# Optimization experiments

Measured on AMD Instinct MI355X. Metric: run time of the kernel, lower is better.

## Reference

```python
import jax, jax.numpy as jnp
import numpy as np

N, V, E_PER = 8, 4608, 73728          # batch, nodes per graph, edges per graph
D_IN, C, NCLS = 1, 512, 3             # node feat dim, embed dim, classes
E = N * E_PER
LN_EPS = 1e-5


def setup_inputs() -> dict:
    key = jax.random.key(0)
    ks = jax.random.split(key, 12)
    x = jax.random.normal(ks[0], (N, 1, V, D_IN), jnp.float32)
    edge_index = jax.random.randint(ks[1], (2, E), 0, V, dtype=jnp.int32)
    edge_weight = jax.random.uniform(ks[2], (E,), jnp.float32)
    # GCNConv params: layer0 maps D_IN->C, layers 1..2 map C->C (weight [in,out], bias [out])
    w0 = jax.random.normal(ks[3], (D_IN, C), jnp.float32) * 0.02
    b0 = jnp.zeros((C,), jnp.float32)
    w1 = jax.random.normal(ks[4], (C, C), jnp.float32) * 0.02
    b1 = jnp.zeros((C,), jnp.float32)
    w2 = jax.random.normal(ks[5], (C, C), jnp.float32) * 0.02
    b2 = jnp.zeros((C,), jnp.float32)
    ln_g = jnp.ones((C,), jnp.float32)
    ln_b = jnp.zeros((C,), jnp.float32)
    head_w = jax.random.normal(ks[6], (C, NCLS), jnp.float32) * 2e-5
    head_b = jnp.log(jnp.full((NCLS,), 1.0 / NCLS, jnp.float32))
    return {"x": x, "edge_weight": edge_weight, "w0": w0, "b0": b0,
            "w1": w1, "b1": b1, "w2": w2, "b2": b2,
            "ln_g": ln_g, "ln_b": ln_b, "head_w": head_w, "head_b": head_b,
            "edge_index": edge_index}


def layer_norm(h, g, b):
    mu = h.mean(-1, keepdims=True)
    var = ((h - mu) ** 2).mean(-1, keepdims=True)
    return (h - mu) * jax.lax.rsqrt(var + LN_EPS) * g + b


def reference(x, edge_weight, w0, b0, w1, b1, w2, b2, ln_g, ln_b, head_w, head_b, edge_index):
    n, t, v, d = x.shape
    nv = n * v
    h = x.reshape(nv, d)
    # batch-offset local edge indices (edges are contiguous per graph)
    offs = jnp.repeat(jnp.arange(n, dtype=edge_index.dtype) * v, edge_index.shape[1] // n)
    src = edge_index[0] + offs
    tgt = edge_index[1] + offs
    # GCN norm with self-loops (fill weight 1.0), symmetric deg^-1/2 normalization
    loop = jnp.arange(nv, dtype=src.dtype)
    src_f = jnp.concatenate([src, loop])
    tgt_f = jnp.concatenate([tgt, loop])
    ew_f = jnp.concatenate([edge_weight, jnp.ones((nv,), edge_weight.dtype)])
    deg = jax.ops.segment_sum(ew_f, tgt_f, num_segments=nv)
    deg_safe = jnp.where(deg > 0, deg, 1.0)
    dinv = jnp.where(deg > 0, jax.lax.rsqrt(deg_safe), 0.0)
    norm = dinv[src_f] * ew_f * dinv[tgt_f]
    for w, bb in ((w0, b0), (w1, b1), (w2, b2)):
        hw = h @ w                                   # [NV, C]
        msg = norm[:, None] * hw[src_f]              # gather + scale  [E+NV, C]
        h = jax.ops.segment_sum(msg, tgt_f, num_segments=nv) + bb
        h = jax.nn.relu(h)
        h = layer_norm(h, ln_g, ln_b)
        # dropout is identity in eval mode
    pooled = h.reshape(n, v, -1).max(axis=1)         # global_max_pool (contiguous batch)
    pooled = layer_norm(pooled, ln_g, ln_b)
    return pooled @ head_w + head_b                  # [N, NCLS]
```

## Files before the change

kernel.cpp:

```cpp
#include <hip/hip_runtime.h>
#include <hip/hip_bf16.h>
#include <stdint.h>

#define N_GRAPH 8
#define V_NODES 4608
#define E_PER   73728
#define NV      (N_GRAPH * V_NODES)
#define E_TOT   (N_GRAPH * E_PER)
#define C       512
#define NCLS    3
#define LN_EPS  1e-5f
#define POOL_CHUNKS 36
#define POOL_PARTS  144
#define SCAN_BLOCKS 144
#define SUBB    32
#define EPSB    (E_PER / SUBB)

typedef __attribute__((ext_vector_type(8))) short short8;
typedef __attribute__((ext_vector_type(4))) float floatx4;
typedef __attribute__((ext_vector_type(2))) float float2v;
typedef __attribute__((address_space(1))) void v_g;
typedef __attribute__((address_space(3))) void v_l;


__device__ inline float waveReduceSum(float v) {
#pragma unroll
    for (int o = 32; o > 0; o >>= 1) v += __shfl_down(v, o, 64);
    return v;
}

__device__ inline float waveAllSum(float v) {
#pragma unroll
    for (int o = 32; o > 0; o >>= 1) v += __shfl_xor(v, o, 64);
    return v;
}

__device__ inline float blockSum512(float v, volatile float* sred) {
    float s = waveReduceSum(v);
    if ((threadIdx.x & 63) == 0) sred[threadIdx.x >> 6] = s;
    __syncthreads();
    float t = 0.f;
#pragma unroll
    for (int i = 0; i < 8; i++) t += sred[i];
    __syncthreads();
    return t;
}

__device__ inline unsigned short f2bf(float f) {
    uint32_t u = __float_as_uint(f);
    u += 0x7fffu + ((u >> 16) & 1u);
    return (unsigned short)(u >> 16);
}
__device__ inline float bf2f(unsigned short b) {
    return __uint_as_float(((uint32_t)b) << 16);
}


#if __has_builtin(__builtin_amdgcn_cvt_pk_fp8_f32)
__device__ inline uint32_t pk_fp8(float a, float b) {
    return (uint32_t)__builtin_amdgcn_cvt_pk_fp8_f32(a, b, 0, false);
}
#else
__device__ inline uint32_t fp8_enc1(float f) {
    float a = fminf(fmaxf(f, -448.f), 448.f);
    uint32_t u = __float_as_uint(a);
    uint32_t s = (u >> 24) & 0x80;
    int e = (int)((u >> 23) & 0xff) - 127;
    uint32_t m = u & 0x7fffff;
    if (a == 0.f || e < -9) return s;
    if (e < -6) {
        int sh = -6 - e;
        uint32_t full = 0x800000u | m;
        uint32_t q = full >> (20 + sh);
        uint32_t rem = full & ((1u << (20 + sh)) - 1);
        uint32_t half = 1u << (19 + sh);
        q += (rem > half || (rem == half && (q & 1)));
        return s | q;
    }
    uint32_t q = m >> 20;
    uint32_t rem = m & 0xfffff;
    q += (rem > 0x80000 || (rem == 0x80000 && (q & 1)));
    uint32_t v = ((uint32_t)(e + 7) << 3) + q;
    if (v > 0x7e) v = 0x7e;
    return s | v;
}
__device__ inline uint32_t pk_fp8(float a, float b) {
    return fp8_enc1(a) | (fp8_enc1(b) << 8);
}
#endif

#if __has_builtin(__builtin_amdgcn_cvt_pk_f32_fp8)
__device__ inline float2v up_fp8_lo(uint32_t w) { return __builtin_amdgcn_cvt_pk_f32_fp8((int)w, false); }
__device__ inline float2v up_fp8_hi(uint32_t w) { return __builtin_amdgcn_cvt_pk_f32_fp8((int)w, true); }
#else
__device__ inline float fp8_dec1(uint32_t b) {
    uint32_t s = (b >> 7) & 1u, e = (b >> 3) & 0xfu, m = b & 7u;
    float mag = e ? ldexpf(1.0f + (float)m * 0.125f, (int)e - 7)
                  : (float)m * 0.001953125f;
    return s ? -mag : mag;
}
__device__ inline float2v up_fp8_lo(uint32_t w) {
    float2v r; r.x = fp8_dec1(w & 0xff); r.y = fp8_dec1((w >> 8) & 0xff); return r;
}
__device__ inline float2v up_fp8_hi(uint32_t w) {
    float2v r; r.x = fp8_dec1((w >> 16) & 0xff); r.y = fp8_dec1(w >> 24); return r;
}
#endif


__launch_bounds__(256)
__global__ void k_hist(const int* __restrict__ ei, const float* __restrict__ ew,
                       int* __restrict__ hist_c, float* __restrict__ hist_d) {
    __shared__ int   lcnt[V_NODES];
    __shared__ float ldeg[V_NODES];
    const int g = blockIdx.x >> 5, j = blockIdx.x & 31;
    const int tid = threadIdx.x;
    for (int i = tid; i < V_NODES; i += 256) { lcnt[i] = 0; ldeg[i] = 0.f; }
    __syncthreads();
    const int ebase = g * E_PER + j * EPSB;
    const int*   tgt = ei + E_TOT + ebase;
    const float* w   = ew + ebase;
    for (int i = tid; i < EPSB; i += 256) {
        int t = tgt[i];
        atomicAdd(&lcnt[t], 1);
        atomicAdd(&ldeg[t], w[i]);
    }
    __syncthreads();
    const size_t hb = ((size_t)g * SUBB + j) * V_NODES;
    for (int i = tid; i < V_NODES; i += 256) {
        hist_c[hb + i] = lcnt[i];
        hist_d[hb + i] = ldeg[i];
    }
}

__global__ void k_reduce(int* __restrict__ hist_c, const float* __restrict__ hist_d,
                         int* __restrict__ counts, float* __restrict__ dinv) {
    const int node = blockIdx.x * 256 + threadIdx.x;
    if (node >= NV) return;
    const int g = node / V_NODES, t = node - g * V_NODES;
    const size_t base = (size_t)g * SUBB * V_NODES + t;
    int c = 0;
    float d = 1.0f;
#pragma unroll 8
    for (int j = 0; j < SUBB; j++) {
        const size_t idx = base + (size_t)j * V_NODES;
        int cc = hist_c[idx];
        hist_c[idx] = c;
        c += cc;
        d += hist_d[idx];
    }
    counts[node] = c;
    dinv[node] = rsqrtf(d);
}


__global__ void k_scan1(const int* __restrict__ counts, int* __restrict__ row_ptr,
                        int* __restrict__ bsum) {
    __shared__ int sh[256];
    const int b = blockIdx.x, tid = threadIdx.x;
    const int idx = b * 256 + tid;
    int v = counts[idx];
    sh[tid] = v;
    __syncthreads();
#pragma unroll
    for (int off = 1; off < 256; off <<= 1) {
        int t = (tid >= off) ? sh[tid - off] : 0;
        __syncthreads();
        sh[tid] += t;
        __syncthreads();
    }
    row_ptr[idx] = sh[tid] - v;
    if (tid == 255) bsum[b] = sh[255];
}

__global__ void k_scan2(int* __restrict__ bsum) {
    __shared__ int sh[256];
    const int tid = threadIdx.x;
    int v = (tid < SCAN_BLOCKS) ? bsum[tid] : 0;
    sh[tid] = v;
    __syncthreads();
#pragma unroll
    for (int off = 1; off < 256; off <<= 1) {
        int t = (tid >= off) ? sh[tid - off] : 0;
        __syncthreads();
        sh[tid] += t;
        __syncthreads();
    }
    if (tid < SCAN_BLOCKS) bsum[tid] = sh[tid] - v;
}

__global__ void k_scan3(int* __restrict__ row_ptr, const int* __restrict__ bsum) {
    const int b = blockIdx.x, tid = threadIdx.x;
    const int idx = b * 256 + tid;
    row_ptr[idx] += bsum[b];
    if (idx == 0) row_ptr[NV] = E_TOT;
}

__launch_bounds__(256)
__global__ void k_fill2(const int* __restrict__ ei, const float* __restrict__ ew,
                        const float* __restrict__ dinv, const int* __restrict__ row_ptr,
                        const int* __restrict__ hist_c, const float* __restrict__ x,
                        int* __restrict__ col_idx, float* __restrict__ val,
                        float* __restrict__ hist_s) {
    __shared__ int   cur[V_NODES];
    __shared__ float sacc[V_NODES];
    const int g = blockIdx.x >> 5, j = blockIdx.x & 31;
    const int tid = threadIdx.x;
    const int gV = g * V_NODES;
    const size_t hb = ((size_t)g * SUBB + j) * V_NODES;
    for (int i = tid; i < V_NODES; i += 256) {
        cur[i] = row_ptr[gV + i] + hist_c[hb + i];
        sacc[i] = 0.f;
    }
    __syncthreads();
    const int ebase = g * E_PER + j * EPSB;
    const int*   src = ei + ebase;
    const int*   tgt = ei + E_TOT + ebase;
    const float* w   = ew + ebase;
    for (int i = tid; i < EPSB; i += 256) {
        int t = tgt[i];
        int s = src[i] + gV;
        float v = dinv[s] * w[i] * dinv[gV + t];
        int pos = atomicAdd(&cur[t], 1);
        col_idx[pos] = s;
        val[pos] = v;
        atomicAdd(&sacc[t], v * x[s]);
    }
    __syncthreads();
    for (int i = tid; i < V_NODES; i += 256)
        hist_s[hb + i] = sacc[i];
}


__global__ void k_wt(const float* __restrict__ w1, const float* __restrict__ w2,
                     unsigned short* __restrict__ wt1, unsigned short* __restrict__ wt2) {
    int idx = blockIdx.x * 256 + threadIdx.x;
    int which = idx >> 18;
    int rem = idx & 0x3ffff;
    int n = rem >> 9, k = rem & 511;
    const float* W = which ? w2 : w1;
    unsigned short* WT = which ? wt2 : wt1;
    WT[n * C + k] = f2bf(W[k * C + n]);
}


__launch_bounds__(128)
__global__ void k_l0post(const float* __restrict__ x, const float* __restrict__ dinv,
                         const float* __restrict__ hist_s,
                         const float* __restrict__ w0, const float* __restrict__ b0,
                         const float* __restrict__ ln_g, const float* __restrict__ ln_b,
                         unsigned short* __restrict__ out) {
    const int node = blockIdx.x;
    const int tid = threadIdx.x;
    const int g = node / V_NODES, t = node - g * V_NODES;
    __shared__ float s_sh;
    if (tid < 32) {
        float p = hist_s[((size_t)g * SUBB + tid) * V_NODES + t];
#pragma unroll
        for (int o = 16; o > 0; o >>= 1) p += __shfl_xor(p, o, 32);
        if (tid == 0) {
            float dt = dinv[node];
            s_sh = dt * dt * x[node] + p;
        }
    }
    __syncthreads();
    const float s = s_sh;
    const int c4 = tid << 2;
    float4 w = *reinterpret_cast<const float4*>(&w0[c4]);
    float4 bb = *reinterpret_cast<const float4*>(&b0[c4]);
    float vx = fmaxf(s * w.x + bb.x, 0.f);
    float vy = fmaxf(s * w.y + bb.y, 0.f);
    float vz = fmaxf(s * w.z + bb.z, 0.f);
    float vw = fmaxf(s * w.w + bb.w, 0.f);
    __shared__ float redA[2], redB[2];
    float wsum = waveReduceSum(vx + vy + vz + vw);
    if ((tid & 63) == 0) redA[tid >> 6] = wsum;
    __syncthreads();
    float mu = (redA[0] + redA[1]) * (1.0f / C);
    float dx = vx - mu, dy = vy - mu, dz = vz - mu, dw = vw - mu;
    float wsq = waveReduceSum(dx * dx + dy * dy + dz * dz + dw * dw);
    if ((tid & 63) == 0) redB[tid >> 6] = wsq;
    __syncthreads();
    float rstd = rsqrtf((redB[0] + redB[1]) * (1.0f / C) + LN_EPS);
    float4 gg = *reinterpret_cast<const float4*>(&ln_g[c4]);
    float4 b = *reinterpret_cast<const float4*>(&ln_b[c4]);
    ushort4 o = { f2bf(dx * rstd * gg.x + b.x), f2bf(dy * rstd * gg.y + b.y),
                  f2bf(dz * rstd * gg.z + b.z), f2bf(dw * rstd * gg.w + b.w) };
    reinterpret_cast<ushort4*>(out)[(size_t)node * 128 + tid] = o;
}


__launch_bounds__(256)
__global__ void k_gemm_mfma(const unsigned short* __restrict__ A,
                            const unsigned short* __restrict__ WT,
                            uint8_t* __restrict__ Bout) {
    __shared__ short8 lA[512];
    __shared__ short8 lB[512];
    const int tid = threadIdx.x;
    const int lane = tid & 63;
    const int wave = tid >> 6;
    const int wr = wave >> 1, wc = wave & 1;
    const int l15 = lane & 15, kg = lane >> 4;
    const int m0 = blockIdx.x * 128;
    const int n0 = blockIdx.y * 128;

    floatx4 acc[4][4] = {};

    const int s0i = tid, s1i = 256 + tid;
    const int kgs0 = s0i >> 7, idx0 = s0i & 127;
    const int kgs1 = s1i >> 7, idx1 = s1i & 127;
    const unsigned short* gA0 = A + (size_t)(m0 + idx0) * C + kgs0 * 8;
    const unsigned short* gA1 = A + (size_t)(m0 + idx1) * C + kgs1 * 8;
    const unsigned short* gB0 = WT + (size_t)(n0 + idx0) * C + kgs0 * 8;
    const unsigned short* gB1 = WT + (size_t)(n0 + idx1) * C + kgs1 * 8;

    for (int k0 = 0; k0 < C; k0 += 32) {
        __builtin_amdgcn_global_load_lds((v_g*)(gA0 + k0), (v_l*)&lA[s0i], 16, 0, 0);
        __builtin_amdgcn_global_load_lds((v_g*)(gA1 + k0), (v_l*)&lA[s1i], 16, 0, 0);
        __builtin_amdgcn_global_load_lds((v_g*)(gB0 + k0), (v_l*)&lB[s0i], 16, 0, 0);
        __builtin_amdgcn_global_load_lds((v_g*)(gB1 + k0), (v_l*)&lB[s1i], 16, 0, 0);
        asm volatile("s_waitcnt vmcnt(0)" ::: "memory");
        __syncthreads();

        short8 af[4], bf[4];
#pragma unroll
        for (int mi = 0; mi < 4; mi++)
            af[mi] = lA[kg * 128 + wr * 64 + mi * 16 + l15];
#pragma unroll
        for (int ni = 0; ni < 4; ni++)
            bf[ni] = lB[kg * 128 + wc * 64 + ni * 16 + l15];
#pragma unroll
        for (int mi = 0; mi < 4; mi++)
#pragma unroll
            for (int ni = 0; ni < 4; ni++)
                acc[mi][ni] = __builtin_amdgcn_mfma_f32_16x16x32_bf16(
                    af[mi], bf[ni], acc[mi][ni], 0, 0, 0);
        __syncthreads();
    }

#pragma unroll
    for (int mi = 0; mi < 4; mi++) {
#pragma unroll
        for (int ni = 0; ni < 4; ni++) {
            int n = n0 + wc * 64 + ni * 16 + l15;
            floatx4 v = acc[mi][ni];
            uint32_t p01 = pk_fp8(v[0], v[1]);
            uint32_t p23 = pk_fp8(v[2], v[3]);
            uint8_t* rp = Bout + (size_t)(m0 + wr * 64 + mi * 16 + kg * 4) * C + n;
            rp[0]     = (uint8_t)p01;
            rp[C]     = (uint8_t)(p01 >> 8);
            rp[2 * C] = (uint8_t)p23;
            rp[3 * C] = (uint8_t)(p23 >> 8);
        }
    }
}


__launch_bounds__(256)
__global__ void k_agg(const uint8_t* __restrict__ hw, const int* __restrict__ row_ptr,
                      const int* __restrict__ col_idx, const float* __restrict__ val,
                      const float* __restrict__ dinv, const float* __restrict__ bias,
                      const float* __restrict__ ln_g, const float* __restrict__ ln_b,
                      unsigned short* __restrict__ out) {
    const int b = blockIdx.x;
    const int wv = threadIdx.x >> 6;
    const int lane = threadIdx.x & 63;
    const int t = (b & 7) * V_NODES + ((b >> 3) << 2) + wv;
    const int e0 = row_ptr[t], e1 = row_ptr[t + 1];
    const uint2* hw8 = reinterpret_cast<const uint2*>(hw);

    const float dt = dinv[t];
    const float selfw = dt * dt;
    float a[8];
    {
        uint2 hv = hw8[(size_t)t * 64 + lane];
        float2v f01 = up_fp8_lo(hv.x), f23 = up_fp8_hi(hv.x);
        float2v f45 = up_fp8_lo(hv.y), f67 = up_fp8_hi(hv.y);
        a[0] = selfw * f01.x; a[1] = selfw * f01.y;
        a[2] = selfw * f23.x; a[3] = selfw * f23.y;
        a[4] = selfw * f45.x; a[5] = selfw * f45.y;
        a[6] = selfw * f67.x; a[7] = selfw * f67.y;
    }

    int e = e0;
    for (; e + 4 <= e1; e += 4) {
        int i0 = col_idx[e], i1 = col_idx[e + 1], i2 = col_idx[e + 2], i3 = col_idx[e + 3];
        float w0 = val[e], w1 = val[e + 1], w2 = val[e + 2], w3 = val[e + 3];
        uint2 h0 = hw8[(size_t)i0 * 64 + lane];
        uint2 h1 = hw8[(size_t)i1 * 64 + lane];
        uint2 h2 = hw8[(size_t)i2 * 64 + lane];
        uint2 h3 = hw8[(size_t)i3 * 64 + lane];
#define ACC8(hv, w) { \
        float2v q01 = up_fp8_lo(hv.x), q23 = up_fp8_hi(hv.x); \
        float2v q45 = up_fp8_lo(hv.y), q67 = up_fp8_hi(hv.y); \
        a[0] += (w) * q01.x; a[1] += (w) * q01.y; \
        a[2] += (w) * q23.x; a[3] += (w) * q23.y; \
        a[4] += (w) * q45.x; a[5] += (w) * q45.y; \
        a[6] += (w) * q67.x; a[7] += (w) * q67.y; }
        ACC8(h0, w0) ACC8(h1, w1) ACC8(h2, w2) ACC8(h3, w3)
    }
    for (; e < e1; e++) {
        int is = col_idx[e];
        float w = val[e];
        uint2 hv = hw8[(size_t)is * 64 + lane];
        ACC8(hv, w)
    }
#undef ACC8

    const int c8 = lane << 3;
    float4 bb0 = *reinterpret_cast<const float4*>(&bias[c8]);
    float4 bb1 = *reinterpret_cast<const float4*>(&bias[c8 + 4]);
    a[0] = fmaxf(a[0] + bb0.x, 0.f); a[1] = fmaxf(a[1] + bb0.y, 0.f);
    a[2] = fmaxf(a[2] + bb0.z, 0.f); a[3] = fmaxf(a[3] + bb0.w, 0.f);
    a[4] = fmaxf(a[4] + bb1.x, 0.f); a[5] = fmaxf(a[5] + bb1.y, 0.f);
    a[6] = fmaxf(a[6] + bb1.z, 0.f); a[7] = fmaxf(a[7] + bb1.w, 0.f);

    float s = a[0] + a[1] + a[2] + a[3] + a[4] + a[5] + a[6] + a[7];
    float mu = waveAllSum(s) * (1.0f / C);
    float sq = 0.f;
#pragma unroll
    for (int i = 0; i < 8; i++) { float d = a[i] - mu; sq += d * d; }
    float rstd = rsqrtf(waveAllSum(sq) * (1.0f / C) + LN_EPS);

    float4 g0 = *reinterpret_cast<const float4*>(&ln_g[c8]);
    float4 g1 = *reinterpret_cast<const float4*>(&ln_g[c8 + 4]);
    float4 z0 = *reinterpret_cast<const float4*>(&ln_b[c8]);
    float4 z1 = *reinterpret_cast<const float4*>(&ln_b[c8 + 4]);
    short8 o;
    o[0] = (short)f2bf((a[0] - mu) * rstd * g0.x + z0.x);
    o[1] = (short)f2bf((a[1] - mu) * rstd * g0.y + z0.y);
    o[2] = (short)f2bf((a[2] - mu) * rstd * g0.z + z0.z);
    o[3] = (short)f2bf((a[3] - mu) * rstd * g0.w + z0.w);
    o[4] = (short)f2bf((a[4] - mu) * rstd * g1.x + z1.x);
    o[5] = (short)f2bf((a[5] - mu) * rstd * g1.y + z1.y);
    o[6] = (short)f2bf((a[6] - mu) * rstd * g1.z + z1.z);
    o[7] = (short)f2bf((a[7] - mu) * rstd * g1.w + z1.w);
    reinterpret_cast<short8*>(out)[(size_t)t * 64 + lane] = o;
}


__launch_bounds__(256)
__global__ void k_pool1(const unsigned short* __restrict__ h, float* __restrict__ pmax) {
    const int g = blockIdx.x, chunk = blockIdx.y;
    const int wv = threadIdx.x >> 6, lane = threadIdx.x & 63;
    const short8* h8 = reinterpret_cast<const short8*>(h);
    const size_t r0 = (size_t)g * V_NODES + chunk * 128 + wv * 32;
    float m[8];
#pragma unroll
    for (int i = 0; i < 8; i++) m[i] = -1e30f;
    for (int r = 0; r < 32; r++) {
        short8 v = h8[(r0 + r) * 64 + lane];
#pragma unroll
        for (int i = 0; i < 8; i++) m[i] = fmaxf(m[i], bf2f((unsigned short)v[i]));
    }
    float* dst = pmax + ((size_t)(g * POOL_PARTS + chunk * 4 + wv)) * C + (lane << 3);
    float4 o0 = { m[0], m[1], m[2], m[3] };
    float4 o1 = { m[4], m[5], m[6], m[7] };
    *reinterpret_cast<float4*>(dst) = o0;
    *reinterpret_cast<float4*>(dst + 4) = o1;
}

__global__ void k_pool2_head(const float* __restrict__ pmax, const float* __restrict__ ln_g,
                             const float* __restrict__ ln_b, const float* __restrict__ hw,
                             const float* __restrict__ hb, float* __restrict__ out) {
    __shared__ float sred[8];
    int g = blockIdx.x;
    int c = threadIdx.x;
    float m = -1e30f;
    for (int j = 0; j < POOL_PARTS; j++)
        m = fmaxf(m, pmax[((size_t)g * POOL_PARTS + j) * C + c]);
    float total = blockSum512(m, sred);
    float mu = total * (1.0f / C);
    float d = m - mu;
    float var = blockSum512(d * d, sred) * (1.0f / C);
    float rstd = rsqrtf(var + LN_EPS);
    float p = d * rstd * ln_g[c] + ln_b[c];
    float r0 = blockSum512(p * hw[c * NCLS + 0], sred);
    float r1 = blockSum512(p * hw[c * NCLS + 1], sred);
    float r2 = blockSum512(p * hw[c * NCLS + 2], sred);
    if (threadIdx.x == 0) {
        out[g * NCLS + 0] = r0 + hb[0];
        out[g * NCLS + 1] = r1 + hb[1];
        out[g * NCLS + 2] = r2 + hb[2];
    }
}


extern "C" void kernel_launch(void* const* d_in, const int* in_sizes, int n_in,
                              void* d_out, int out_size, void* d_ws, size_t ws_size,
                              hipStream_t stream) {
    const float* x      = (const float*)d_in[0];
    const float* ew     = (const float*)d_in[1];
    const float* w0     = (const float*)d_in[2];
    const float* b0     = (const float*)d_in[3];
    const float* w1     = (const float*)d_in[4];
    const float* b1     = (const float*)d_in[5];
    const float* w2     = (const float*)d_in[6];
    const float* b2     = (const float*)d_in[7];
    const float* ln_g   = (const float*)d_in[8];
    const float* ln_b   = (const float*)d_in[9];
    const float* head_w = (const float*)d_in[10];
    const float* head_b = (const float*)d_in[11];
    const int*   ei     = (const int*)d_in[12];
    float* out = (float*)d_out;

    char* p = (char*)d_ws;
    auto alloc = [&](size_t bytes) { void* r = p; p += (bytes + 255) & ~255ull; return r; };
    unsigned short* bufA = (unsigned short*)alloc((size_t)NV * C * 2);
    uint8_t*        bufF = (uint8_t*)alloc((size_t)NV * C);
    unsigned short* wt1  = (unsigned short*)alloc((size_t)C * C * 2);
    unsigned short* wt2  = (unsigned short*)alloc((size_t)C * C * 2);
    float* dinv    = (float*)alloc((size_t)NV * 4);
    int*   counts  = (int*)alloc((size_t)NV * 4);
    int*   row_ptr = (int*)alloc((size_t)(NV + 1) * 4);
    int*   bsum    = (int*)alloc((size_t)SCAN_BLOCKS * 4);
    int*   hist_c  = (int*)alloc((size_t)N_GRAPH * SUBB * V_NODES * 4);
    float* hist_d  = (float*)alloc((size_t)N_GRAPH * SUBB * V_NODES * 4);
    int*   col_idx = (int*)alloc((size_t)E_TOT * 4);
    float* val     = (float*)alloc((size_t)E_TOT * 4);
    float* pmax    = (float*)alloc((size_t)N_GRAPH * POOL_PARTS * C * 4);

    k_hist<<<N_GRAPH * SUBB, 256, 0, stream>>>(ei, ew, hist_c, hist_d);
    k_reduce<<<SCAN_BLOCKS, 256, 0, stream>>>(hist_c, hist_d, counts, dinv);
    k_scan1<<<SCAN_BLOCKS, 256, 0, stream>>>(counts, row_ptr, bsum);
    k_scan2<<<1, 256, 0, stream>>>(bsum);
    k_scan3<<<SCAN_BLOCKS, 256, 0, stream>>>(row_ptr, bsum);
    k_fill2<<<N_GRAPH * SUBB, 256, 0, stream>>>(ei, ew, dinv, row_ptr, hist_c, x,
                                                col_idx, val, hist_d);
    k_wt<<<(2 * C * C) / 256, 256, 0, stream>>>(w1, w2, wt1, wt2);

    k_l0post<<<NV, 128, 0, stream>>>(x, dinv, hist_d, w0, b0, ln_g, ln_b, bufA);

    k_gemm_mfma<<<dim3(NV / 128, C / 128), 256, 0, stream>>>(bufA, wt1, bufF);
    k_agg<<<NV / 4, 256, 0, stream>>>(bufF, row_ptr, col_idx, val, dinv, b1, ln_g, ln_b, bufA);

    k_gemm_mfma<<<dim3(NV / 128, C / 128), 256, 0, stream>>>(bufA, wt2, bufF);
    k_agg<<<NV / 4, 256, 0, stream>>>(bufF, row_ptr, col_idx, val, dinv, b2, ln_g, ln_b, bufA);

    k_pool1<<<dim3(N_GRAPH, POOL_CHUNKS), 256, 0, stream>>>(bufA, pmax);
    k_pool2_head<<<N_GRAPH, C, 0, stream>>>(pmax, ln_g, ln_b, head_w, head_b, out);
}
```

Measured before the change: 368.8 us.

## Fuse reduce with block scan, deepen GEMM K-tile, unroll aggregation gathers by eight

Result: slower. 379.4 us (+2.9%).

```diff
diff --git a/kernel.cpp b/kernel.cpp
--- a/kernel.cpp
+++ b/kernel.cpp
@@ -133,10 +133,13 @@
     }
 }
 
-__global__ void k_reduce(int* __restrict__ hist_c, const float* __restrict__ hist_d,
-                         int* __restrict__ counts, float* __restrict__ dinv) {
-    const int node = blockIdx.x * 256 + threadIdx.x;
-    if (node >= NV) return;
+__launch_bounds__(256)
+__global__ void k_reduce_scan(int* __restrict__ hist_c, const float* __restrict__ hist_d,
+                              float* __restrict__ dinv, int* __restrict__ row_ptr,
+                              int* __restrict__ bsum) {
+    __shared__ int sh[256];
+    const int tid = threadIdx.x;
+    const int node = blockIdx.x * 256 + tid;
     const int g = node / V_NODES, t = node - g * V_NODES;
     const size_t base = (size_t)g * SUBB * V_NODES + t;
     int c = 0;
@@ -149,28 +152,18 @@
         c += cc;
         d += hist_d[idx];
     }
-    counts[node] = c;
     dinv[node] = rsqrtf(d);
-}
-
-
-__global__ void k_scan1(const int* __restrict__ counts, int* __restrict__ row_ptr,
-                        int* __restrict__ bsum) {
-    __shared__ int sh[256];
-    const int b = blockIdx.x, tid = threadIdx.x;
-    const int idx = b * 256 + tid;
-    int v = counts[idx];
-    sh[tid] = v;
+    sh[tid] = c;
     __syncthreads();
 #pragma unroll
     for (int off = 1; off < 256; off <<= 1) {
-        int t = (tid >= off) ? sh[tid - off] : 0;
+        int v = (tid >= off) ? sh[tid - off] : 0;
         __syncthreads();
-        sh[tid] += t;
+        sh[tid] += v;
         __syncthreads();
     }
-    row_ptr[idx] = sh[tid] - v;
-    if (tid == 255) bsum[b] = sh[255];
+    row_ptr[node] = sh[tid] - c;
+    if (tid == 255) bsum[blockIdx.x] = sh[255];
 }
 
 __global__ void k_scan2(int* __restrict__ bsum) {
@@ -294,8 +287,8 @@
 __global__ void k_gemm_mfma(const unsigned short* __restrict__ A,
                             const unsigned short* __restrict__ WT,
                             uint8_t* __restrict__ Bout) {
-    __shared__ short8 lA[512];
-    __shared__ short8 lB[512];
+    __shared__ short8 lA[1024];
+    __shared__ short8 lB[1024];
     const int tid = threadIdx.x;
     const int lane = tid & 63;
     const int wave = tid >> 6;
@@ -306,35 +299,41 @@
 
     floatx4 acc[4][4] = {};
 
-    const int s0i = tid, s1i = 256 + tid;
-    const int kgs0 = s0i >> 7, idx0 = s0i & 127;
-    const int kgs1 = s1i >> 7, idx1 = s1i & 127;
-    const unsigned short* gA0 = A + (size_t)(m0 + idx0) * C + kgs0 * 8;
-    const unsigned short* gA1 = A + (size_t)(m0 + idx1) * C + kgs1 * 8;
-    const unsigned short* gB0 = WT + (size_t)(n0 + idx0) * C + kgs0 * 8;
-    const unsigned short* gB1 = WT + (size_t)(n0 + idx1) * C + kgs1 * 8;
-
-    for (int k0 = 0; k0 < C; k0 += 32) {
-        __builtin_amdgcn_global_load_lds((v_g*)(gA0 + k0), (v_l*)&lA[s0i], 16, 0, 0);
-        __builtin_amdgcn_global_load_lds((v_g*)(gA1 + k0), (v_l*)&lA[s1i], 16, 0, 0);
-        __builtin_amdgcn_global_load_lds((v_g*)(gB0 + k0), (v_l*)&lB[s0i], 16, 0, 0);
-        __builtin_amdgcn_global_load_lds((v_g*)(gB1 + k0), (v_l*)&lB[s1i], 16, 0, 0);
+    const unsigned short* gA[4];
+    const unsigned short* gB[4];
+#pragma unroll
+    for (int i = 0; i < 4; i++) {
+        int s = i * 256 + tid;
+        int kc = s >> 7, row = s & 127;
+        gA[i] = A  + (size_t)(m0 + row) * C + kc * 8;
+        gB[i] = WT + (size_t)(n0 + row) * C + kc * 8;
+    }
+
+    for (int k0 = 0; k0 < C; k0 += 64) {
+#pragma unroll
+        for (int i = 0; i < 4; i++) {
+            __builtin_amdgcn_global_load_lds((v_g*)(gA[i] + k0), (v_l*)&lA[i * 256 + tid], 16, 0, 0);
+            __builtin_amdgcn_global_load_lds((v_g*)(gB[i] + k0), (v_l*)&lB[i * 256 + tid], 16, 0, 0);
+        }
         asm volatile("s_waitcnt vmcnt(0)" ::: "memory");
         __syncthreads();
 
-        short8 af[4], bf[4];
-#pragma unroll
-        for (int mi = 0; mi < 4; mi++)
-            af[mi] = lA[kg * 128 + wr * 64 + mi * 16 + l15];
-#pragma unroll
-        for (int ni = 0; ni < 4; ni++)
-            bf[ni] = lB[kg * 128 + wc * 64 + ni * 16 + l15];
-#pragma unroll
-        for (int mi = 0; mi < 4; mi++)
+#pragma unroll
+        for (int ks = 0; ks < 2; ks++) {
+            short8 af[4], bf[4];
+#pragma unroll
+            for (int mi = 0; mi < 4; mi++)
+                af[mi] = lA[(ks * 4 + kg) * 128 + wr * 64 + mi * 16 + l15];
 #pragma unroll
             for (int ni = 0; ni < 4; ni++)
-                acc[mi][ni] = __builtin_amdgcn_mfma_f32_16x16x32_bf16(
-                    af[mi], bf[ni], acc[mi][ni], 0, 0, 0);
+                bf[ni] = lB[(ks * 4 + kg) * 128 + wc * 64 + ni * 16 + l15];
+#pragma unroll
+            for (int mi = 0; mi < 4; mi++)
+#pragma unroll
+                for (int ni = 0; ni < 4; ni++)
+                    acc[mi][ni] = __builtin_amdgcn_mfma_f32_16x16x32_bf16(
+                        af[mi], bf[ni], acc[mi][ni], 0, 0, 0);
+        }
         __syncthreads();
     }
 
@@ -382,14 +381,6 @@
         a[6] = selfw * f67.x; a[7] = selfw * f67.y;
     }
 
-    int e = e0;
-    for (; e + 4 <= e1; e += 4) {
-        int i0 = col_idx[e], i1 = col_idx[e + 1], i2 = col_idx[e + 2], i3 = col_idx[e + 3];
-        float w0 = val[e], w1 = val[e + 1], w2 = val[e + 2], w3 = val[e + 3];
-        uint2 h0 = hw8[(size_t)i0 * 64 + lane];
-        uint2 h1 = hw8[(size_t)i1 * 64 + lane];
-        uint2 h2 = hw8[(size_t)i2 * 64 + lane];
-        uint2 h3 = hw8[(size_t)i3 * 64 + lane];
 #define ACC8(hv, w) { \
         float2v q01 = up_fp8_lo(hv.x), q23 = up_fp8_hi(hv.x); \
         float2v q45 = up_fp8_lo(hv.y), q67 = up_fp8_hi(hv.y); \
@@ -397,12 +388,33 @@
         a[2] += (w) * q23.x; a[3] += (w) * q23.y; \
         a[4] += (w) * q45.x; a[5] += (w) * q45.y; \
         a[6] += (w) * q67.x; a[7] += (w) * q67.y; }
-        ACC8(h0, w0) ACC8(h1, w1) ACC8(h2, w2) ACC8(h3, w3)
+
+    int e = e0;
+    for (; e + 8 <= e1; e += 8) {
+        uint2 h[8];
+        float w[8];
+#pragma unroll
+        for (int q = 0; q < 8; q++) {
+            h[q] = hw8[(size_t)col_idx[e + q] * 64 + lane];
+            w[q] = val[e + q];
+        }
+#pragma unroll
+        for (int q = 0; q < 8; q++) ACC8(h[q], w[q])
+    }
+    for (; e + 4 <= e1; e += 4) {
+        uint2 h[4];
+        float w[4];
+#pragma unroll
+        for (int q = 0; q < 4; q++) {
+            h[q] = hw8[(size_t)col_idx[e + q] * 64 + lane];
+            w[q] = val[e + q];
+        }
+#pragma unroll
+        for (int q = 0; q < 4; q++) ACC8(h[q], w[q])
     }
     for (; e < e1; e++) {
-        int is = col_idx[e];
+        uint2 hv = hw8[(size_t)col_idx[e] * 64 + lane];
         float w = val[e];
-        uint2 hv = hw8[(size_t)is * 64 + lane];
         ACC8(hv, w)
     }
 #undef ACC8
@@ -511,7 +523,6 @@
     unsigned short* wt1  = (unsigned short*)alloc((size_t)C * C * 2);
     unsigned short* wt2  = (unsigned short*)alloc((size_t)C * C * 2);
     float* dinv    = (float*)alloc((size_t)NV * 4);
-    int*   counts  = (int*)alloc((size_t)NV * 4);
     int*   row_ptr = (int*)alloc((size_t)(NV + 1) * 4);
     int*   bsum    = (int*)alloc((size_t)SCAN_BLOCKS * 4);
     int*   hist_c  = (int*)alloc((size_t)N_GRAPH * SUBB * V_NODES * 4);
@@ -521,8 +532,7 @@
     float* pmax    = (float*)alloc((size_t)N_GRAPH * POOL_PARTS * C * 4);
 
     k_hist<<<N_GRAPH * SUBB, 256, 0, stream>>>(ei, ew, hist_c, hist_d);
-    k_reduce<<<SCAN_BLOCKS, 256, 0, stream>>>(hist_c, hist_d, counts, dinv);
-    k_scan1<<<SCAN_BLOCKS, 256, 0, stream>>>(counts, row_ptr, bsum);
+    k_reduce_scan<<<SCAN_BLOCKS, 256, 0, stream>>>(hist_c, hist_d, dinv, row_ptr, bsum);
     k_scan2<<<1, 256, 0, stream>>>(bsum);
     k_scan3<<<SCAN_BLOCKS, 256, 0, stream>>>(row_ptr, bsum);
     k_fill2<<<N_GRAPH * SUBB, 256, 0, stream>>>(ei, ew, dinv, row_ptr, hist_c, x,
```
